# Kernel tuning notes

Hardware: AMD Instinct MI355X
Metric: run time of the kernel (lower is better)

Reference implementation:

```python
import jax, jax.numpy as jnp
import numpy as np

B, S, D, H, DFF = 4, 2048, 1024, 16, 4096
DK = D // H
EPS = 1e-6


def layernorm(x, w, b):
    # Faithful to source: unbiased std (ddof=1), divides by (std + eps).
    mean = jnp.mean(x, axis=-1, keepdims=True)
    std = jnp.std(x, axis=-1, keepdims=True, ddof=1)
    return w * (x - mean) / (std + EPS) + b


def setup_inputs() -> dict:
    key = jax.random.key(0)
    ks = jax.random.split(key, 16)
    g = lambda k, shape: (jax.random.normal(k, shape, dtype=jnp.float32) * 0.02)
    inp = {
        "x": jax.random.normal(ks[0], (B, S, D), dtype=jnp.float32),
        "mask": jnp.ones((B, 1, 1, S), dtype=jnp.int32),
        # attention projections (stored [in, out]; math identical to torch Linear)
        "wq": g(ks[1], (D, D)), "bq": jnp.zeros((D,), jnp.float32),
        "wk": g(ks[2], (D, D)), "bk": jnp.zeros((D,), jnp.float32),
        "wv": g(ks[3], (D, D)), "bv": jnp.zeros((D,), jnp.float32),
        "wo": g(ks[4], (D, D)), "bo": jnp.zeros((D,), jnp.float32),
        # feed-forward
        "w1": g(ks[5], (D, DFF)), "b1": jnp.zeros((DFF,), jnp.float32),
        "w2": g(ks[6], (DFF, D)), "b2": jnp.zeros((D,), jnp.float32),
        # layer norms
        "ln1_w": jnp.ones((D,), jnp.float32), "ln1_b": jnp.zeros((D,), jnp.float32),
        "ln2_w": jnp.ones((D,), jnp.float32), "ln2_b": jnp.zeros((D,), jnp.float32),
    }
    return inp


def attention(xn, mask, wq, bq, wk, bk, wv, bv, wo, bo):
    q = (xn @ wq + bq).reshape(B, S, H, DK)
    k = (xn @ wk + bk).reshape(B, S, H, DK)
    v = (xn @ wv + bv).reshape(B, S, H, DK)
    scores = jnp.einsum("bqhd,bkhd->bhqk", q, k) / jnp.sqrt(jnp.float32(DK))
    scores = jnp.where(mask == 0, -jnp.inf, scores)
    attn = jax.nn.softmax(scores, axis=-1)  # dropout identity at inference
    out = jnp.einsum("bhqk,bkhd->bqhd", attn, v).reshape(B, S, D)
    return out @ wo + bo


def reference(x, mask, wq, bq, wk, bk, wv, bv, wo, bo,
              w1, b1, w2, b2, ln1_w, ln1_b, ln2_w, ln2_b):
    # pre-norm residual 1: self-attention
    x = x + attention(layernorm(x, ln1_w, ln1_b), mask,
                      wq, bq, wk, bk, wv, bv, wo, bo)
    # pre-norm residual 2: FFN
    xn = layernorm(x, ln2_w, ln2_b)
    ffn = jax.nn.relu(xn @ w1 + b1) @ w2 + b2
    return x + ffn
```

## Files before the change

kernel.cpp:

```cpp
#include <hip/hip_runtime.h>


typedef unsigned short u16;
typedef unsigned u32;
typedef __bf16 bf16x8 __attribute__((ext_vector_type(8)));
typedef float f32x4 __attribute__((ext_vector_type(4)));
typedef float f32x16 __attribute__((ext_vector_type(16)));

typedef __attribute__((address_space(1))) const void* as1_cvp;
typedef __attribute__((address_space(3))) void* as3_vp;

__device__ __forceinline__ void async_copy16(const void* g, void* l) {
  __builtin_amdgcn_global_load_lds((as1_cvp)g, (as3_vp)l, 16, 0, 0);
}

__device__ __forceinline__ u16 f2bf(float f) {
  unsigned u = __float_as_uint(f);
  u += 0x7fffu + ((u >> 16) & 1u);
  return (u16)(u >> 16);
}

__device__ __forceinline__ float fast_exp2(float x) {
  return __builtin_amdgcn_exp2f(x);
}

__device__ __forceinline__ u32 cvt_pk_bf16(float lo, float hi) {
  u32 d;
  asm("v_cvt_pk_bf16_f32 %0, %1, %2" : "=v"(d) : "v"(lo), "v"(hi));
  return d;
}

__device__ __forceinline__ void permlane32_swap(u32& x, u32& y) {
  asm volatile("v_permlane32_swap_b32 %0, %1" : "+v"(x), "+v"(y));
}

__global__ __launch_bounds__(256) void k_transpose_bf16(
    const float* __restrict__ src, u16* __restrict__ dst, int K, int N,
    float scale) {
  __shared__ float tile[32][33];
  int n0 = blockIdx.x * 32, k0 = blockIdx.y * 32;
  int c = threadIdx.x & 31, r0 = threadIdx.x >> 5;
#pragma unroll
  for (int i = 0; i < 32; i += 8)
    tile[r0 + i][c] = src[(size_t)(k0 + r0 + i) * N + n0 + c];
  __syncthreads();
#pragma unroll
  for (int i = 0; i < 32; i += 8)
    dst[(size_t)(n0 + r0 + i) * K + k0 + c] = f2bf(tile[c][r0 + i] * scale);
}

__global__ __launch_bounds__(256) void k_pack_bias(
    const float* __restrict__ bq, const float* __restrict__ bk,
    const float* __restrict__ bv, float* __restrict__ out, float qscale) {
  int i = blockIdx.x * 256 + threadIdx.x;
  float v;
  if (i < 1024) v = bq[i] * qscale;
  else if (i < 2048) v = bk[i - 1024];
  else v = bv[i - 2048];
  out[i] = v;
}

__global__ __launch_bounds__(256) void k_maskadd(
    const int* __restrict__ mask, float* __restrict__ madd) {
  int i = blockIdx.x * 256 + threadIdx.x;
  madd[i] = mask[i] ? 0.0f : -1e30f;
}

__global__ __launch_bounds__(256) void k_layernorm_bf16(
    const float* __restrict__ x, const float* __restrict__ w,
    const float* __restrict__ b, u16* __restrict__ out) {
  const int D = 1024;
  int row = blockIdx.x, tid = threadIdx.x;
  const float4* xr = (const float4*)(x + (size_t)row * D);
  float4 v = xr[tid];
  float s = v.x + v.y + v.z + v.w;
  float ss = v.x * v.x + v.y * v.y + v.z * v.z + v.w * v.w;
#pragma unroll
  for (int off = 1; off < 64; off <<= 1) {
    s += __shfl_xor(s, off);
    ss += __shfl_xor(ss, off);
  }
  __shared__ float rs[4], rss[4];
  int wave = tid >> 6, lane = tid & 63;
  if (lane == 0) { rs[wave] = s; rss[wave] = ss; }
  __syncthreads();
  float S_ = rs[0] + rs[1] + rs[2] + rs[3];
  float SS = rss[0] + rss[1] + rss[2] + rss[3];
  float mean = S_ * (1.0f / D);
  float var = (SS - (float)D * mean * mean) * (1.0f / (D - 1));
  float inv = 1.0f / (sqrtf(fmaxf(var, 0.0f)) + 1e-6f);
  float4 wv = ((const float4*)w)[tid], bv = ((const float4*)b)[tid];
  u16* orow = out + (size_t)row * D + tid * 4;
  orow[0] = f2bf(wv.x * (v.x - mean) * inv + bv.x);
  orow[1] = f2bf(wv.y * (v.y - mean) * inv + bv.y);
  orow[2] = f2bf(wv.z * (v.z - mean) * inv + bv.z);
  orow[3] = f2bf(wv.w * (v.w - mean) * inv + bv.w);
}

template <bool RELU, bool HAS_RES, bool OUT_BF16>
__global__ __launch_bounds__(512, 2) void k_gemm2(
    const u16* __restrict__ A, const u16* __restrict__ Bt,
    const float* __restrict__ bias, const float* __restrict__ res,
    void* __restrict__ outp, int M, int N, int K) {
  __shared__ __align__(16) u16 lds[3 * 24576];
  const int tid = threadIdx.x;
  const int lane = tid & 63, wave = tid >> 6;
  const int quad = lane >> 4, l16 = lane & 15;
  const int m0 = blockIdx.x * 256, n0 = blockIdx.y * 128;
  const int wm = (wave >> 1) * 64, wn = (wave & 1) * 64;

  const int srow = tid >> 3;
  const int schunk8 = ((tid & 7) ^ (srow & 7)) * 8;
  const u16* gA0 = A + (size_t)(m0 + srow) * K + schunk8;
  const u16* gA1 = A + (size_t)(m0 + 64 + srow) * K + schunk8;
  const u16* gA2 = A + (size_t)(m0 + 128 + srow) * K + schunk8;
  const u16* gA3 = A + (size_t)(m0 + 192 + srow) * K + schunk8;
  const u16* gB0 = Bt + (size_t)(n0 + srow) * K + schunk8;
  const u16* gB1 = Bt + (size_t)(n0 + 64 + srow) * K + schunk8;

  auto STAGE = [&](int t, int s) {
    const size_t ko = (size_t)t * 64;
    u16* sb = lds + s * 24576;
    async_copy16(gA0 + ko, sb + tid * 8);
    async_copy16(gA1 + ko, sb + 4096 + tid * 8);
    async_copy16(gA2 + ko, sb + 8192 + tid * 8);
    async_copy16(gA3 + ko, sb + 12288 + tid * 8);
    async_copy16(gB0 + ko, sb + 16384 + tid * 8);
    async_copy16(gB1 + ko, sb + 20480 + tid * 8);
  };

  f32x4 zero = {0.0f, 0.0f, 0.0f, 0.0f};
  f32x4 acc[4][4];
#pragma unroll
  for (int i = 0; i < 4; i++)
#pragma unroll
    for (int j = 0; j < 4; j++) acc[i][j] = zero;

  STAGE(0, 0);
  STAGE(1, 1);
  const int NT = K >> 6;
  for (int t = 0; t < NT; t++) {
    asm volatile("s_waitcnt vmcnt(6)" ::: "memory");
    __builtin_amdgcn_s_barrier();
    if (t + 2 < NT) STAGE(t + 2, (t + 2) % 3);
    const u16* sb = lds + (t % 3) * 24576;
    const u16* sbB = sb + 16384;
#pragma unroll
    for (int ks = 0; ks < 2; ks++) {
      bf16x8 af[4], bfr[4];
#pragma unroll
      for (int mb = 0; mb < 4; mb++) {
        int R = wm + mb * 16 + l16;
        af[mb] = *(const bf16x8*)&sb[R * 64 + (((4 * ks + quad) ^ (R & 7)) * 8)];
      }
#pragma unroll
      for (int nb = 0; nb < 4; nb++) {
        int C = wn + nb * 16 + l16;
        bfr[nb] =
            *(const bf16x8*)&sbB[C * 64 + (((4 * ks + quad) ^ (C & 7)) * 8)];
      }
#pragma unroll
      for (int mb = 0; mb < 4; mb++)
#pragma unroll
        for (int nb = 0; nb < 4; nb++)
          acc[mb][nb] = __builtin_amdgcn_mfma_f32_16x16x32_bf16(
              af[mb], bfr[nb], acc[mb][nb], 0, 0, 0);
    }
  }
#pragma unroll
  for (int mb = 0; mb < 4; mb++) {
#pragma unroll
    for (int nb = 0; nb < 4; nb++) {
      int col = n0 + wn + nb * 16 + l16;
      float bb = bias[col];
#pragma unroll
      for (int r = 0; r < 4; r++) {
        int row = m0 + wm + mb * 16 + quad * 4 + r;
        float vv = acc[mb][nb][r] + bb;
        if (HAS_RES) vv += res[(size_t)row * N + col];
        if (RELU) vv = fmaxf(vv, 0.0f);
        if (OUT_BF16) ((u16*)outp)[(size_t)row * N + col] = f2bf(vv);
        else ((float*)outp)[(size_t)row * N + col] = vv;
      }
    }
  }
}

__global__ __launch_bounds__(512, 4) void k_attention(
    const u16* __restrict__ qkv, const float* __restrict__ madd,
    u16* __restrict__ out) {
  const int S = 2048, D = 1024, QS = 3072;
  int blk = blockIdx.x;
  int xcd = blk & 7, t = blk >> 3;
  int qt = t & 7, gg = t >> 3;
  int g = gg * 8 + xcd;
  int h = g & 15, bb = g >> 4;
  int tid = threadIdx.x, lane = tid & 63, wave = tid >> 6;
  int l32 = lane & 31, hh = lane >> 5;

  __shared__ __align__(16) u16 Ks[64 * 64];
  __shared__ __align__(16) u16 Vs[64 * 64];

  const int qrowbase = bb * S + qt * 256;
  const int sbase = bb * S;
  const int qrow = qrowbase + wave * 32 + l32;

  bf16x8 qf[4];
  {
    const u16* qp = qkv + (size_t)qrow * QS + h * 64 + 8 * hh;
#pragma unroll
    for (int c = 0; c < 4; c++) qf[c] = *(const bf16x8*)(qp + 16 * c);
  }

  bf16x8 ones;
  {
    union { u16 s[8]; bf16x8 v; } o_;
#pragma unroll
    for (int j = 0; j < 8; j++) o_.s[j] = 0x3F80;
    ones = o_.v;
  }

  f32x16 accA, accB, lacc;
#pragma unroll
  for (int r = 0; r < 16; r++) { accA[r] = 0.0f; accB[r] = 0.0f; lacc[r] = 0.0f; }

  const int krow = tid >> 3, ko = ((tid & 7) ^ (krow & 7)) * 8;
  const int vkey = tid >> 3, vf = tid & 7;

  for (int kt = 0; kt < 32; kt++) {
    const int kb0 = sbase + kt * 64;
    __syncthreads();
    async_copy16(qkv + (size_t)(kb0 + krow) * QS + 1024 + h * 64 + ko,
                 Ks + tid * 8);
    {
      union { uint4 u; u16 s[8]; } tt;
      tt.u = *(const uint4*)(qkv + (size_t)(kb0 + vkey) * QS + 2048 + h * 64 +
                             vf * 8);
#pragma unroll
      for (int j = 0; j < 8; j++)
        Vs[(8 * vf + j) * 64 + (vkey ^ (8 * (vf ^ j)))] = tt.s[j];
    }
    __syncthreads();

    u32 pa[4][4];
#pragma unroll
    for (int kb = 0; kb < 2; kb++) {
      const int kr = kb * 32 + l32;
      f32x16 sc;
#pragma unroll
      for (int r = 0; r < 16; r++) sc[r] = 0.0f;
#pragma unroll
      for (int c = 0; c < 4; c++) {
        bf16x8 kf = *(const bf16x8*)&Ks[kr * 64 + (((2 * c + hh) ^ (kr & 7)) * 8)];
        sc = __builtin_amdgcn_mfma_f32_32x32x16_bf16(kf, qf[c], sc, 0, 0, 0);
      }
      f32x4 mv0 = *(const f32x4*)(madd + kb0 + kb * 32 + 0 + 4 * hh);
      f32x4 mv1 = *(const f32x4*)(madd + kb0 + kb * 32 + 8 + 4 * hh);
      f32x4 mv2 = *(const f32x4*)(madd + kb0 + kb * 32 + 16 + 4 * hh);
      f32x4 mv3 = *(const f32x4*)(madd + kb0 + kb * 32 + 24 + 4 * hh);
#pragma unroll
      for (int r = 0; r < 4; r++) sc[r] = fast_exp2(sc[r] + mv0[r]);
#pragma unroll
      for (int r = 0; r < 4; r++) sc[4 + r] = fast_exp2(sc[4 + r] + mv1[r]);
#pragma unroll
      for (int r = 0; r < 4; r++) sc[8 + r] = fast_exp2(sc[8 + r] + mv2[r]);
#pragma unroll
      for (int r = 0; r < 4; r++) sc[12 + r] = fast_exp2(sc[12 + r] + mv3[r]);
#pragma unroll
      for (int hk = 0; hk < 2; hk++) {
        u32 a0 = cvt_pk_bf16(sc[hk * 8 + 0], sc[hk * 8 + 1]);
        u32 a1 = cvt_pk_bf16(sc[hk * 8 + 2], sc[hk * 8 + 3]);
        u32 b0 = cvt_pk_bf16(sc[hk * 8 + 4], sc[hk * 8 + 5]);
        u32 b1 = cvt_pk_bf16(sc[hk * 8 + 6], sc[hk * 8 + 7]);
        permlane32_swap(a0, b0);
        permlane32_swap(a1, b1);
        pa[kb * 2 + hk][0] = a0;
        pa[kb * 2 + hk][1] = a1;
        pa[kb * 2 + hk][2] = b0;
        pa[kb * 2 + hk][3] = b1;
      }
    }
#pragma unroll
    for (int kc = 0; kc < 4; kc++) {
      union { u32 u[4]; bf16x8 v; } pu;
      pu.u[0] = pa[kc][0]; pu.u[1] = pa[kc][1];
      pu.u[2] = pa[kc][2]; pu.u[3] = pa[kc][3];
      lacc = __builtin_amdgcn_mfma_f32_32x32x16_bf16(pu.v, ones, lacc, 0, 0, 0);
      const int kch = 2 * kc + hh;
      const int r0v = l32;
      bf16x8 v0 =
          *(const bf16x8*)&Vs[r0v * 64 + ((kch ^ (((r0v >> 3) ^ r0v) & 7)) * 8)];
      accA = __builtin_amdgcn_mfma_f32_32x32x16_bf16(pu.v, v0, accA, 0, 0, 0);
      const int r1v = 32 + l32;
      bf16x8 v1 =
          *(const bf16x8*)&Vs[r1v * 64 + ((kch ^ (((r1v >> 3) ^ r1v) & 7)) * 8)];
      accB = __builtin_amdgcn_mfma_f32_32x32x16_bf16(pu.v, v1, accB, 0, 0, 0);
    }
  }
#pragma unroll
  for (int r = 0; r < 16; r++) {
    float inv = 1.0f / lacc[r];
    size_t row = (size_t)(qrowbase + wave * 32 + (r & 3) + 8 * (r >> 2) + 4 * hh);
    u16* op = out + row * D + h * 64;
    op[l32] = f2bf(accA[r] * inv);
    op[32 + l32] = f2bf(accB[r] * inv);
  }
}

extern "C" void kernel_launch(void* const* d_in, const int* in_sizes, int n_in,
                              void* d_out, int out_size, void* d_ws,
                              size_t ws_size, hipStream_t stream) {
  const float* x    = (const float*)d_in[0];
  const int*   mask = (const int*)d_in[1];
  const float* wq = (const float*)d_in[2];   const float* bq = (const float*)d_in[3];
  const float* wk = (const float*)d_in[4];   const float* bk = (const float*)d_in[5];
  const float* wv = (const float*)d_in[6];   const float* bv = (const float*)d_in[7];
  const float* wo = (const float*)d_in[8];   const float* bo = (const float*)d_in[9];
  const float* w1 = (const float*)d_in[10];  const float* b1 = (const float*)d_in[11];
  const float* w2 = (const float*)d_in[12];  const float* b2 = (const float*)d_in[13];
  const float* ln1w = (const float*)d_in[14]; const float* ln1b = (const float*)d_in[15];
  const float* ln2w = (const float*)d_in[16]; const float* ln2b = (const float*)d_in[17];
  float* outp = (float*)d_out;

  char* ws = (char*)d_ws;
  const size_t MB = 1024 * 1024;
  u16* wqkvT = (u16*)(ws + 0 * MB);
  u16* woT   = (u16*)(ws + 6 * MB);
  u16* w1T   = (u16*)(ws + 8 * MB);
  u16* w2T   = (u16*)(ws + 16 * MB);
  u16* xn    = (u16*)(ws + 24 * MB);
  u16* qkvb  = (u16*)(ws + 40 * MB);
  u16* hb    = (u16*)(ws + 40 * MB);
  float* bqkv = (float*)(ws + 88 * MB);
  float* madd = (float*)(ws + 88 * MB + 64 * 1024);
  float* y1  = (float*)(ws + 104 * MB);

  const float qscale = 0.125f * 1.44269504f;

  k_transpose_bf16<<<dim3(32, 32), 256, 0, stream>>>(wq, wqkvT, 1024, 1024, qscale);
  k_transpose_bf16<<<dim3(32, 32), 256, 0, stream>>>(wk, wqkvT + 1024 * 1024, 1024, 1024, 1.0f);
  k_transpose_bf16<<<dim3(32, 32), 256, 0, stream>>>(wv, wqkvT + 2048 * 1024, 1024, 1024, 1.0f);
  k_transpose_bf16<<<dim3(32, 32), 256, 0, stream>>>(wo, woT, 1024, 1024, 1.0f);
  k_transpose_bf16<<<dim3(128, 32), 256, 0, stream>>>(w1, w1T, 1024, 4096, 1.0f);
  k_transpose_bf16<<<dim3(32, 128), 256, 0, stream>>>(w2, w2T, 4096, 1024, 1.0f);
  k_pack_bias<<<12, 256, 0, stream>>>(bq, bk, bv, bqkv, qscale);
  k_maskadd<<<32, 256, 0, stream>>>(mask, madd);

  k_layernorm_bf16<<<8192, 256, 0, stream>>>(x, ln1w, ln1b, xn);

  k_gemm2<false, false, true><<<dim3(32, 24), 512, 0, stream>>>(
      xn, wqkvT, bqkv, nullptr, qkvb, 8192, 3072, 1024);

  k_attention<<<512, 512, 0, stream>>>(qkvb, madd, xn);

  dim3 go(32, 8);
  k_gemm2<false, true, false><<<go, 512, 0, stream>>>(xn, woT, bo, x, y1, 8192, 1024, 1024);

  k_layernorm_bf16<<<8192, 256, 0, stream>>>(y1, ln2w, ln2b, xn);

  k_gemm2<true, false, true><<<dim3(32, 32), 512, 0, stream>>>(
      xn, w1T, b1, nullptr, hb, 8192, 4096, 1024);

  k_gemm2<false, true, false><<<go, 512, 0, stream>>>(hb, w2T, b2, y1, outp, 8192, 1024, 4096);
}
```

Baseline: 500.6 us.

## Double-buffer K/V tiles in attention and stage mask row in LDS

The attention kernel now uses two LDS buffers for K and V and prefetches the next key tile into registers (V) and LDS (K, via async copy) while computing on the current tile. Explicit waitcnt plus a single barrier replace the two __syncthreads per iteration. The whole mask-add row for the batch is copied into LDS once up front instead of being read from global memory every tile. This aims to hide global load latency behind MFMA work, at the cost of more LDS per block, which may lower occupancy, and fragile hand-written waitcnt counts.

```diff
diff --git a/kernel.cpp b/kernel.cpp
--- a/kernel.cpp
+++ b/kernel.cpp
@@ -191,15 +191,16 @@
     u16* __restrict__ out) {
   const int S = 2048, D = 1024, QS = 3072;
   int blk = blockIdx.x;
-  int xcd = blk & 7, t = blk >> 3;
-  int qt = t & 7, gg = t >> 3;
+  int xcd = blk & 7, t0 = blk >> 3;
+  int qt = t0 & 7, gg = t0 >> 3;
   int g = gg * 8 + xcd;
   int h = g & 15, bb = g >> 4;
   int tid = threadIdx.x, lane = tid & 63, wave = tid >> 6;
   int l32 = lane & 31, hh = lane >> 5;
 
-  __shared__ __align__(16) u16 Ks[64 * 64];
-  __shared__ __align__(16) u16 Vs[64 * 64];
+  __shared__ __align__(16) u16 Ks[2][64 * 64];
+  __shared__ __align__(16) u16 Vs[2][64 * 64];
+  __shared__ __align__(16) float Ms[2048];
 
   const int qrowbase = bb * S + qt * 256;
   const int sbase = bb * S;
@@ -227,20 +228,33 @@
   const int krow = tid >> 3, ko = ((tid & 7) ^ (krow & 7)) * 8;
   const int vkey = tid >> 3, vf = tid & 7;
 
-  for (int kt = 0; kt < 32; kt++) {
-    const int kb0 = sbase + kt * 64;
-    __syncthreads();
-    async_copy16(qkv + (size_t)(kb0 + krow) * QS + 1024 + h * 64 + ko,
-                 Ks + tid * 8);
+  uint4 vbc, vbn;
+
+  vbc = *(const uint4*)(qkv + (size_t)(sbase + vkey) * QS + 2048 + h * 64 +
+                        vf * 8);
+  async_copy16(madd + sbase + tid * 4, Ms + tid * 4);
+  async_copy16(qkv + (size_t)(sbase + krow) * QS + 1024 + h * 64 + ko,
+               Ks[0] + tid * 8);
+
+  auto STEP = [&](int t, u16* KsC, u16* KsN, u16* VsC, uint4& vbU, uint4& vbL,
+                  bool last) {
+    if (!last) {
+      const int nb0 = sbase + (t + 1) * 64;
+      vbL = *(const uint4*)(qkv + (size_t)(nb0 + vkey) * QS + 2048 + h * 64 +
+                            vf * 8);
+      async_copy16(qkv + (size_t)(nb0 + krow) * QS + 1024 + h * 64 + ko,
+                   KsN + tid * 8);
+    }
     {
-      union { uint4 u; u16 s[8]; } tt;
-      tt.u = *(const uint4*)(qkv + (size_t)(kb0 + vkey) * QS + 2048 + h * 64 +
-                             vf * 8);
+      union { uint4 u; u16 s[8]; } tv;
+      tv.u = vbU;
 #pragma unroll
       for (int j = 0; j < 8; j++)
-        Vs[(8 * vf + j) * 64 + (vkey ^ (8 * (vf ^ j)))] = tt.s[j];
-    }
-    __syncthreads();
+        VsC[(8 * vf + j) * 64 + (vkey ^ (8 * (vf ^ j)))] = tv.s[j];
+    }
+    if (!last) asm volatile("s_waitcnt vmcnt(2) lgkmcnt(0)" ::: "memory");
+    else       asm volatile("s_waitcnt vmcnt(0) lgkmcnt(0)" ::: "memory");
+    __builtin_amdgcn_s_barrier();
 
     u32 pa[4][4];
 #pragma unroll
@@ -251,13 +265,14 @@
       for (int r = 0; r < 16; r++) sc[r] = 0.0f;
 #pragma unroll
       for (int c = 0; c < 4; c++) {
-        bf16x8 kf = *(const bf16x8*)&Ks[kr * 64 + (((2 * c + hh) ^ (kr & 7)) * 8)];
+        bf16x8 kf =
+            *(const bf16x8*)&KsC[kr * 64 + (((2 * c + hh) ^ (kr & 7)) * 8)];
         sc = __builtin_amdgcn_mfma_f32_32x32x16_bf16(kf, qf[c], sc, 0, 0, 0);
       }
-      f32x4 mv0 = *(const f32x4*)(madd + kb0 + kb * 32 + 0 + 4 * hh);
-      f32x4 mv1 = *(const f32x4*)(madd + kb0 + kb * 32 + 8 + 4 * hh);
-      f32x4 mv2 = *(const f32x4*)(madd + kb0 + kb * 32 + 16 + 4 * hh);
-      f32x4 mv3 = *(const f32x4*)(madd + kb0 + kb * 32 + 24 + 4 * hh);
+      f32x4 mv0 = *(const f32x4*)&Ms[t * 64 + kb * 32 + 0 + 4 * hh];
+      f32x4 mv1 = *(const f32x4*)&Ms[t * 64 + kb * 32 + 8 + 4 * hh];
+      f32x4 mv2 = *(const f32x4*)&Ms[t * 64 + kb * 32 + 16 + 4 * hh];
+      f32x4 mv3 = *(const f32x4*)&Ms[t * 64 + kb * 32 + 24 + 4 * hh];
 #pragma unroll
       for (int r = 0; r < 4; r++) sc[r] = fast_exp2(sc[r] + mv0[r]);
 #pragma unroll
@@ -289,18 +304,27 @@
       const int kch = 2 * kc + hh;
       const int r0v = l32;
       bf16x8 v0 =
-          *(const bf16x8*)&Vs[r0v * 64 + ((kch ^ (((r0v >> 3) ^ r0v) & 7)) * 8)];
+          *(const bf16x8*)&VsC[r0v * 64 + ((kch ^ (((r0v >> 3) ^ r0v) & 7)) * 8)];
       accA = __builtin_amdgcn_mfma_f32_32x32x16_bf16(pu.v, v0, accA, 0, 0, 0);
       const int r1v = 32 + l32;
       bf16x8 v1 =
-          *(const bf16x8*)&Vs[r1v * 64 + ((kch ^ (((r1v >> 3) ^ r1v) & 7)) * 8)];
+          *(const bf16x8*)&VsC[r1v * 64 + ((kch ^ (((r1v >> 3) ^ r1v) & 7)) * 8)];
       accB = __builtin_amdgcn_mfma_f32_32x32x16_bf16(pu.v, v1, accB, 0, 0, 0);
     }
-  }
+    __builtin_amdgcn_s_barrier();
+  };
+
+#pragma unroll 1
+  for (int tt = 0; tt < 16; tt++) {
+    STEP(2 * tt, Ks[0], Ks[1], Vs[0], vbc, vbn, false);
+    STEP(2 * tt + 1, Ks[1], Ks[0], Vs[1], vbn, vbc, tt == 15);
+  }
+
 #pragma unroll
   for (int r = 0; r < 16; r++) {
     float inv = 1.0f / lacc[r];
-    size_t row = (size_t)(qrowbase + wave * 32 + (r & 3) + 8 * (r >> 2) + 4 * hh);
+    size_t row =
+        (size_t)(qrowbase + wave * 32 + (r & 3) + 8 * (r >> 2) + 4 * hh);
     u16* op = out + row * D + h * 64;
     op[l32] = f2bf(accA[r] * inv);
     op[32 + l32] = f2bf(accB[r] * inv);
```

Measured after the change: 507.6 us. No clear change (+1.4%).

## Process two query subtiles per wave in attention, halving block threads

Applied to the files above, without the earlier changes.

The attention kernel now uses 256 threads per block, and each wave handles 64 query rows as two 32-row subtiles. Each K and V fragment read from LDS is reused across both subtiles. The mask-add vector for the batch is preloaded once into shared memory instead of being read from global memory every iteration. This doubles the accumulator registers per wave and lowers the number of waves per block, which risks lower occupancy and less latency hiding.

```diff
diff --git a/kernel.cpp b/kernel.cpp
--- a/kernel.cpp
+++ b/kernel.cpp
@@ -186,13 +186,13 @@
   }
 }
 
-__global__ __launch_bounds__(512, 4) void k_attention(
+__global__ __launch_bounds__(256, 2) void k_attention(
     const u16* __restrict__ qkv, const float* __restrict__ madd,
     u16* __restrict__ out) {
   const int S = 2048, D = 1024, QS = 3072;
   int blk = blockIdx.x;
-  int xcd = blk & 7, t = blk >> 3;
-  int qt = t & 7, gg = t >> 3;
+  int xcd = blk & 7, t0 = blk >> 3;
+  int qt = t0 & 7, gg = t0 >> 3;
   int g = gg * 8 + xcd;
   int h = g & 15, bb = g >> 4;
   int tid = threadIdx.x, lane = tid & 63, wave = tid >> 6;
@@ -200,16 +200,21 @@
 
   __shared__ __align__(16) u16 Ks[64 * 64];
   __shared__ __align__(16) u16 Vs[64 * 64];
+  __shared__ __align__(16) float Ms[2048];
 
   const int qrowbase = bb * S + qt * 256;
   const int sbase = bb * S;
-  const int qrow = qrowbase + wave * 32 + l32;
-
-  bf16x8 qf[4];
+
+  bf16x8 qf0[4], qf1[4];
   {
-    const u16* qp = qkv + (size_t)qrow * QS + h * 64 + 8 * hh;
-#pragma unroll
-    for (int c = 0; c < 4; c++) qf[c] = *(const bf16x8*)(qp + 16 * c);
+    const u16* qp0 =
+        qkv + (size_t)(qrowbase + wave * 64 + l32) * QS + h * 64 + 8 * hh;
+    const u16* qp1 = qp0 + (size_t)32 * QS;
+#pragma unroll
+    for (int c = 0; c < 4; c++) {
+      qf0[c] = *(const bf16x8*)(qp0 + 16 * c);
+      qf1[c] = *(const bf16x8*)(qp1 + 16 * c);
+    }
   }
 
   bf16x8 ones;
@@ -220,90 +225,113 @@
     ones = o_.v;
   }
 
-  f32x16 accA, accB, lacc;
-#pragma unroll
-  for (int r = 0; r < 16; r++) { accA[r] = 0.0f; accB[r] = 0.0f; lacc[r] = 0.0f; }
-
-  const int krow = tid >> 3, ko = ((tid & 7) ^ (krow & 7)) * 8;
-  const int vkey = tid >> 3, vf = tid & 7;
-
+  f32x16 accA0, accB0, lacc0, accA1, accB1, lacc1;
+#pragma unroll
+  for (int r = 0; r < 16; r++) {
+    accA0[r] = 0.0f; accB0[r] = 0.0f; lacc0[r] = 0.0f;
+    accA1[r] = 0.0f; accB1[r] = 0.0f; lacc1[r] = 0.0f;
+  }
+
+  async_copy16(madd + sbase + tid * 4, (float*)Ms + tid * 4);
+  async_copy16(madd + sbase + (tid + 256) * 4, (float*)Ms + (tid + 256) * 4);
+
+#pragma unroll 1
   for (int kt = 0; kt < 32; kt++) {
     const int kb0 = sbase + kt * 64;
     __syncthreads();
-    async_copy16(qkv + (size_t)(kb0 + krow) * QS + 1024 + h * 64 + ko,
-                 Ks + tid * 8);
-    {
-      union { uint4 u; u16 s[8]; } tt;
+#pragma unroll
+    for (int s = 0; s < 2; s++) {
+      int c = tid + s * 256;
+      int krow = c >> 3, ko = ((c & 7) ^ (krow & 7)) * 8;
+      async_copy16(qkv + (size_t)(kb0 + krow) * QS + 1024 + h * 64 + ko,
+                   Ks + c * 8);
+    }
+#pragma unroll
+    for (int s = 0; s < 2; s++) {
+      int jb = tid + s * 256;
+      int vkey = jb >> 3, vf = jb & 7;
+      union { uint4 u; u16 s16[8]; } tt;
       tt.u = *(const uint4*)(qkv + (size_t)(kb0 + vkey) * QS + 2048 + h * 64 +
                              vf * 8);
 #pragma unroll
       for (int j = 0; j < 8; j++)
-        Vs[(8 * vf + j) * 64 + (vkey ^ (8 * (vf ^ j)))] = tt.s[j];
+        Vs[(8 * vf + j) * 64 + (vkey ^ (8 * (vf ^ j)))] = tt.s16[j];
     }
     __syncthreads();
 
-    u32 pa[4][4];
 #pragma unroll
     for (int kb = 0; kb < 2; kb++) {
       const int kr = kb * 32 + l32;
-      f32x16 sc;
-#pragma unroll
-      for (int r = 0; r < 16; r++) sc[r] = 0.0f;
+      bf16x8 kf[4];
+#pragma unroll
+      for (int c = 0; c < 4; c++)
+        kf[c] = *(const bf16x8*)&Ks[kr * 64 + (((2 * c + hh) ^ (kr & 7)) * 8)];
+      f32x16 s0, s1;
+#pragma unroll
+      for (int r = 0; r < 16; r++) { s0[r] = 0.0f; s1[r] = 0.0f; }
 #pragma unroll
       for (int c = 0; c < 4; c++) {
-        bf16x8 kf = *(const bf16x8*)&Ks[kr * 64 + (((2 * c + hh) ^ (kr & 7)) * 8)];
-        sc = __builtin_amdgcn_mfma_f32_32x32x16_bf16(kf, qf[c], sc, 0, 0, 0);
-      }
-      f32x4 mv0 = *(const f32x4*)(madd + kb0 + kb * 32 + 0 + 4 * hh);
-      f32x4 mv1 = *(const f32x4*)(madd + kb0 + kb * 32 + 8 + 4 * hh);
-      f32x4 mv2 = *(const f32x4*)(madd + kb0 + kb * 32 + 16 + 4 * hh);
-      f32x4 mv3 = *(const f32x4*)(madd + kb0 + kb * 32 + 24 + 4 * hh);
-#pragma unroll
-      for (int r = 0; r < 4; r++) sc[r] = fast_exp2(sc[r] + mv0[r]);
-#pragma unroll
-      for (int r = 0; r < 4; r++) sc[4 + r] = fast_exp2(sc[4 + r] + mv1[r]);
-#pragma unroll
-      for (int r = 0; r < 4; r++) sc[8 + r] = fast_exp2(sc[8 + r] + mv2[r]);
-#pragma unroll
-      for (int r = 0; r < 4; r++) sc[12 + r] = fast_exp2(sc[12 + r] + mv3[r]);
+        s0 = __builtin_amdgcn_mfma_f32_32x32x16_bf16(kf[c], qf0[c], s0, 0, 0, 0);
+        s1 = __builtin_amdgcn_mfma_f32_32x32x16_bf16(kf[c], qf1[c], s1, 0, 0, 0);
+      }
+#pragma unroll
+      for (int m = 0; m < 4; m++) {
+        f32x4 mv = *(const f32x4*)&Ms[kt * 64 + kb * 32 + m * 8 + 4 * hh];
+#pragma unroll
+        for (int r = 0; r < 4; r++) {
+          s0[m * 4 + r] = fast_exp2(s0[m * 4 + r] + mv[r]);
+          s1[m * 4 + r] = fast_exp2(s1[m * 4 + r] + mv[r]);
+        }
+      }
 #pragma unroll
       for (int hk = 0; hk < 2; hk++) {
-        u32 a0 = cvt_pk_bf16(sc[hk * 8 + 0], sc[hk * 8 + 1]);
-        u32 a1 = cvt_pk_bf16(sc[hk * 8 + 2], sc[hk * 8 + 3]);
-        u32 b0 = cvt_pk_bf16(sc[hk * 8 + 4], sc[hk * 8 + 5]);
-        u32 b1 = cvt_pk_bf16(sc[hk * 8 + 6], sc[hk * 8 + 7]);
+        u32 a0 = cvt_pk_bf16(s0[hk * 8 + 0], s0[hk * 8 + 1]);
+        u32 a1 = cvt_pk_bf16(s0[hk * 8 + 2], s0[hk * 8 + 3]);
+        u32 b0 = cvt_pk_bf16(s0[hk * 8 + 4], s0[hk * 8 + 5]);
+        u32 b1 = cvt_pk_bf16(s0[hk * 8 + 6], s0[hk * 8 + 7]);
         permlane32_swap(a0, b0);
         permlane32_swap(a1, b1);
-        pa[kb * 2 + hk][0] = a0;
-        pa[kb * 2 + hk][1] = a1;
-        pa[kb * 2 + hk][2] = b0;
-        pa[kb * 2 + hk][3] = b1;
-      }
-    }
-#pragma unroll
-    for (int kc = 0; kc < 4; kc++) {
-      union { u32 u[4]; bf16x8 v; } pu;
-      pu.u[0] = pa[kc][0]; pu.u[1] = pa[kc][1];
-      pu.u[2] = pa[kc][2]; pu.u[3] = pa[kc][3];
-      lacc = __builtin_amdgcn_mfma_f32_32x32x16_bf16(pu.v, ones, lacc, 0, 0, 0);
-      const int kch = 2 * kc + hh;
-      const int r0v = l32;
-      bf16x8 v0 =
-          *(const bf16x8*)&Vs[r0v * 64 + ((kch ^ (((r0v >> 3) ^ r0v) & 7)) * 8)];
-      accA = __builtin_amdgcn_mfma_f32_32x32x16_bf16(pu.v, v0, accA, 0, 0, 0);
-      const int r1v = 32 + l32;
-      bf16x8 v1 =
-          *(const bf16x8*)&Vs[r1v * 64 + ((kch ^ (((r1v >> 3) ^ r1v) & 7)) * 8)];
-      accB = __builtin_amdgcn_mfma_f32_32x32x16_bf16(pu.v, v1, accB, 0, 0, 0);
-    }
-  }
+        union { u32 u[4]; bf16x8 v; } p0;
+        p0.u[0] = a0; p0.u[1] = a1; p0.u[2] = b0; p0.u[3] = b1;
+        u32 c0 = cvt_pk_bf16(s1[hk * 8 + 0], s1[hk * 8 + 1]);
+        u32 c1 = cvt_pk_bf16(s1[hk * 8 + 2], s1[hk * 8 + 3]);
+        u32 d0 = cvt_pk_bf16(s1[hk * 8 + 4], s1[hk * 8 + 5]);
+        u32 d1 = cvt_pk_bf16(s1[hk * 8 + 6], s1[hk * 8 + 7]);
+        permlane32_swap(c0, d0);
+        permlane32_swap(c1, d1);
+        union { u32 u[4]; bf16x8 v; } p1;
+        p1.u[0] = c0; p1.u[1] = c1; p1.u[2] = d0; p1.u[3] = d1;
+
+        const int kc = kb * 2 + hk;
+        const int kch = 2 * kc + hh;
+        lacc0 = __builtin_amdgcn_mfma_f32_32x32x16_bf16(p0.v, ones, lacc0, 0, 0, 0);
+        lacc1 = __builtin_amdgcn_mfma_f32_32x32x16_bf16(p1.v, ones, lacc1, 0, 0, 0);
+        const int r0v = l32;
+        bf16x8 v0 = *(const bf16x8*)&Vs[r0v * 64 +
+                                        ((kch ^ (((r0v >> 3) ^ r0v) & 7)) * 8)];
+        accA0 = __builtin_amdgcn_mfma_f32_32x32x16_bf16(p0.v, v0, accA0, 0, 0, 0);
+        accA1 = __builtin_amdgcn_mfma_f32_32x32x16_bf16(p1.v, v0, accA1, 0, 0, 0);
+        const int r1v = 32 + l32;
+        bf16x8 v1 = *(const bf16x8*)&Vs[r1v * 64 +
+                                        ((kch ^ (((r1v >> 3) ^ r1v) & 7)) * 8)];
+        accB0 = __builtin_amdgcn_mfma_f32_32x32x16_bf16(p0.v, v1, accB0, 0, 0, 0);
+        accB1 = __builtin_amdgcn_mfma_f32_32x32x16_bf16(p1.v, v1, accB1, 0, 0, 0);
+      }
+    }
+  }
+
 #pragma unroll
   for (int r = 0; r < 16; r++) {
-    float inv = 1.0f / lacc[r];
-    size_t row = (size_t)(qrowbase + wave * 32 + (r & 3) + 8 * (r >> 2) + 4 * hh);
-    u16* op = out + row * D + h * 64;
-    op[l32] = f2bf(accA[r] * inv);
-    op[32 + l32] = f2bf(accB[r] * inv);
+    float i0 = 1.0f / lacc0[r];
+    float i1 = 1.0f / lacc1[r];
+    size_t row0 =
+        (size_t)(qrowbase + wave * 64 + (r & 3) + 8 * (r >> 2) + 4 * hh);
+    u16* op0 = out + row0 * D + h * 64;
+    op0[l32] = f2bf(accA0[r] * i0);
+    op0[32 + l32] = f2bf(accB0[r] * i0);
+    u16* op1 = op0 + (size_t)32 * D;
+    op1[l32] = f2bf(accA1[r] * i1);
+    op1[32 + l32] = f2bf(accB1[r] * i1);
   }
 }
 
@@ -351,7 +379,7 @@
   k_gemm2<false, false, true><<<dim3(32, 24), 512, 0, stream>>>(
       xn, wqkvT, bqkv, nullptr, qkvb, 8192, 3072, 1024);
 
-  k_attention<<<512, 512, 0, stream>>>(qkvb, madd, xn);
+  k_attention<<<512, 256, 0, stream>>>(qkvb, madd, xn);
 
   dim3 go(32, 8);
   k_gemm2<false, true, false><<<go, 512, 0, stream>>>(xn, woT, bo, x, y1, 8192, 1024, 1024);
```

New measurement: 482.6 us. 3.6% less time.
